# Optimization experiments

Measured on AMD Instinct MI355X. Metric: run time of the kernel, lower is better.

The kernel has to match this reference:

```python
import jax, jax.numpy as jnp
import numpy as np

ALPHA = 0.3      # robust Welsch scale (hardcoded in calc_chamfer)
EPS = 1e-6       # cosine_similarity eps


def _single_direction(x_points, x_normals, y_points, y_normals):
    """Robust chamfer x->y with K=1 KNN. Returns (mean robust dist, mean normal loss)."""
    # brute-force squared pairwise distances: [B, N, M]
    x2 = jnp.sum(x_points * x_points, axis=-1)            # [B, N]
    y2 = jnp.sum(y_points * y_points, axis=-1)            # [B, M]
    d2 = x2[:, :, None] + y2[:, None, :] - 2.0 * jnp.einsum('bnd,bmd->bnm', x_points, y_points)
    d2 = jnp.maximum(d2, 0.0)
    idx = jnp.argmin(d2, axis=-1)                         # [B, N] nearest neighbor in y
    dists = jnp.take_along_axis(d2, idx[..., None], axis=-1)[..., 0]   # squared dists [B, N]
    # Welsch weight applied to the squared distance (matches torch code), detached
    w = jax.lax.stop_gradient(jnp.exp(-(dists ** 2) / (2.0 * ALPHA * ALPHA)))
    cham_x = jnp.sum(w * dists, axis=1)                   # [B]
    # gather nearest normals and cosine similarity (torch-style per-vector eps clamp)
    yn_near = jnp.take_along_axis(y_normals, idx[..., None], axis=1)   # [B, N, 3]
    xn_norm = jnp.maximum(jnp.linalg.norm(x_normals, axis=-1), EPS)
    yn_norm = jnp.maximum(jnp.linalg.norm(yn_near, axis=-1), EPS)
    cos = jnp.sum(x_normals * yn_near, axis=-1) / (xn_norm * yn_norm)
    cham_norm_x = 1.0 - jnp.abs(cos)                      # abs_cosine=True
    return jnp.mean(cham_x), jnp.mean(cham_norm_x)


def setup_inputs() -> dict:
    key = jax.random.key(0)
    k1, k2, k3, k4 = jax.random.split(key, 4)
    B, N, M = 2, 10000, 10000
    pred_points = jax.random.normal(k1, (B, N, 3), dtype=jnp.float32)
    target_points = jax.random.normal(k2, (B, M, 3), dtype=jnp.float32)
    pn = jax.random.normal(k3, (B, N, 3), dtype=jnp.float32)
    tn = jax.random.normal(k4, (B, M, 3), dtype=jnp.float32)
    pred_normals = pn / jnp.linalg.norm(pn, axis=-1, keepdims=True)
    target_normals = tn / jnp.linalg.norm(tn, axis=-1, keepdims=True)
    return {
        'pred_points': pred_points,
        'pred_normals': pred_normals,
        'target_points': target_points,
        'target_normals': target_normals,
    }


def reference(pred_points, pred_normals, target_points, target_normals):
    # direction 1: target -> pred, direction 2: pred -> target
    d1, n1 = _single_direction(target_points, target_normals, pred_points, pred_normals)
    d2, n2 = _single_direction(pred_points, pred_normals, target_points, target_normals)
    return (d1 + d2, n1 + n2)
```

## Files before the change

### kernel.cpp

```cpp
#include <hip/hip_runtime.h>
#include <math.h>

#define NPTS 10000
#define XPT 8
#define AXCH 5
#define TILE 500

typedef float float2v __attribute__((ext_vector_type(2)));

#define PKFMA(d, a, b, c) \
    asm("v_pk_fma_f32 %0, %1, %2, %3" : "=v"(d) : "v"(a), "v"(b), "v"(c))

__global__ __launch_bounds__(256, 4) void knn_max(
    const float* __restrict__ pred_pts, const float* __restrict__ targ_pts,
    float* __restrict__ wsM, int nslices)
{
    const int slice = NPTS / nslices;
    const int c   = blockIdx.z;
    const int dir = c >> 1, b = c & 1;
    const float* xp = (dir == 0 ? targ_pts : pred_pts) + (size_t)b * NPTS * 3;
    const float* yp = (dir == 0 ? pred_pts : targ_pts) + (size_t)b * NPTS * 3;
    const int s = blockIdx.y;
    const int base = blockIdx.x * (256 * XPT) + threadIdx.x;

    __shared__ float4 spk[TILE];

    float2v xb[4][3];
    float   xs[4][3];
#pragma unroll
    for (int k = 0; k < 8; ++k) {
        const int n = base + k * 256;
        const int nn = (n < NPTS) ? n : (NPTS - 1);
        const float v0 = xp[nn * 3 + 0];
        const float v1 = xp[nn * 3 + 1];
        const float v2 = xp[nn * 3 + 2];
        if (k < 4) {
            xb[k][0] = (float2v){v0, v0};
            xb[k][1] = (float2v){v1, v1};
            xb[k][2] = (float2v){v2, v2};
        } else {
            xs[k - 4][0] = v0; xs[k - 4][1] = v1; xs[k - 4][2] = v2;
        }
    }
    float best[8];
#pragma unroll
    for (int k = 0; k < 8; ++k) best[k] = -1e30f;

    const int jstart = s * slice, jend = jstart + slice;
    for (int t0 = jstart; t0 < jend; t0 += TILE) {
        const int cnt = min(TILE, jend - t0);
        const int np  = cnt >> 1;
        __syncthreads();
        for (int p = threadIdx.x; p < np; p += 256) {
            const int j = t0 + 2 * p;
            const float a0 = yp[j * 3 + 0], b0 = yp[j * 3 + 1], c0 = yp[j * 3 + 2];
            const float a1 = yp[j * 3 + 3], b1 = yp[j * 3 + 4], c1 = yp[j * 3 + 5];
            spk[2 * p]     = make_float4(a0, a1, b0, b1);
            spk[2 * p + 1] = make_float4(c0, c1,
                                         -0.5f * (a0 * a0 + b0 * b0 + c0 * c0),
                                         -0.5f * (a1 * a1 + b1 * b1 + c1 * c1));
        }
        __syncthreads();
#pragma unroll 2
        for (int p = 0; p < np; ++p) {
            const float4 A = spk[2 * p];
            const float4 B = spk[2 * p + 1];
            const float2v px = {A.x, A.y}, py = {A.z, A.w};
            const float2v pz = {B.x, B.y}, pw = {B.z, B.w};
#pragma unroll
            for (int k = 0; k < 4; ++k) {
                float2v t;
                PKFMA(t, xb[k][2], pz, pw);
                PKFMA(t, xb[k][1], py, t);
                PKFMA(t, xb[k][0], px, t);
                best[k] = fmaxf(fmaxf(best[k], t.x), t.y);
            }
#pragma unroll
            for (int k = 0; k < 4; ++k) {
                const float ma = fmaf(xs[k][0], A.x,
                                 fmaf(xs[k][1], A.z, fmaf(xs[k][2], B.x, B.z)));
                const float mb = fmaf(xs[k][0], A.y,
                                 fmaf(xs[k][1], A.w, fmaf(xs[k][2], B.y, B.w)));
                best[4 + k] = fmaxf(fmaxf(best[4 + k], ma), mb);
            }
        }
    }
#pragma unroll
    for (int k = 0; k < 8; ++k) {
        const int n = base + k * 256;
        if (n < NPTS)
            wsM[((size_t)(c * nslices + s)) * NPTS + n] = best[k];
    }
}

__global__ __launch_bounds__(256) void finalize(
    const float* __restrict__ pred_pts, const float* __restrict__ pred_nrm,
    const float* __restrict__ targ_pts, const float* __restrict__ targ_nrm,
    const float* __restrict__ wsM, float2* __restrict__ wsB, int nslices)
{
    const int c   = blockIdx.y;
    const int dir = c >> 1, b = c & 1;
    const float* xp = (dir == 0 ? targ_pts : pred_pts) + (size_t)b * NPTS * 3;
    const float* xn = (dir == 0 ? targ_nrm : pred_nrm) + (size_t)b * NPTS * 3;
    const float* yp = (dir == 0 ? pred_pts : targ_pts) + (size_t)b * NPTS * 3;
    const float* yn = (dir == 0 ? pred_nrm : targ_nrm) + (size_t)b * NPTS * 3;

    const int lane = threadIdx.x & 7;
    const int n = blockIdx.x * 32 + (threadIdx.x >> 3);

    float t0 = 0.f, t1 = 0.f;
    if (n < NPTS) {
        float bm = -1e30f;
        int   bs = 1 << 30;
        for (int s = lane; s < nslices; s += 8) {
            const float m = wsM[((size_t)(c * nslices + s)) * NPTS + n];
            if (m > bm) { bm = m; bs = s; }
        }
#pragma unroll
        for (int w = 1; w < 8; w <<= 1) {
            const float mo = __shfl_xor(bm, w);
            const int   so = __shfl_xor(bs, w);
            if (mo > bm || (mo == bm && so < bs)) { bm = mo; bs = so; }
        }
        const float a  = xp[n * 3 + 0];
        const float bb = xp[n * 3 + 1];
        const float cc = xp[n * 3 + 2];
        const int slice = NPTS / nslices;
        const int j0 = bs * slice;
        float rb = -1e30f;
        int bidx = 1 << 30;
        for (int j = j0 + lane; j < j0 + slice; j += 8) {
            const float ya = yp[j * 3 + 0];
            const float yb = yp[j * 3 + 1];
            const float yc = yp[j * 3 + 2];
            const float hy = -0.5f * (ya * ya + yb * yb + yc * yc);
            const float m  = fmaf(a, ya, fmaf(bb, yb, fmaf(cc, yc, hy)));
            if (m > rb) { rb = m; bidx = j; }
        }
#pragma unroll
        for (int w = 1; w < 8; w <<= 1) {
            const float mo = __shfl_xor(rb, w);
            const int   jo = __shfl_xor(bidx, w);
            if (mo > rb || (mo == rb && jo < bidx)) { rb = mo; bidx = jo; }
        }
        if (lane == 0) {
            const float hx = -0.5f * (a * a + bb * bb + cc * cc);
            float d2 = -2.0f * (rb + hx);
            d2 = fmaxf(d2, 0.0f);
            const float w = __expf(-(d2 * d2) * (1.0f / 0.18f));
            t0 = w * d2;
            const float nx0 = xn[n * 3 + 0], nx1 = xn[n * 3 + 1], nx2 = xn[n * 3 + 2];
            const float ny0 = yn[(size_t)bidx * 3 + 0];
            const float ny1 = yn[(size_t)bidx * 3 + 1];
            const float ny2 = yn[(size_t)bidx * 3 + 2];
            const float nnx = fmaxf(sqrtf(nx0 * nx0 + nx1 * nx1 + nx2 * nx2), 1e-6f);
            const float nny = fmaxf(sqrtf(ny0 * ny0 + ny1 * ny1 + ny2 * ny2), 1e-6f);
            const float cosv = (nx0 * ny0 + nx1 * ny1 + nx2 * ny2) / (nnx * nny);
            t1 = 1.0f - fabsf(cosv);
        }
    }

    __shared__ float r0[256], r1[256];
    r0[threadIdx.x] = t0;
    r1[threadIdx.x] = t1;
    __syncthreads();
    for (int st = 128; st > 0; st >>= 1) {
        if (threadIdx.x < st) {
            r0[threadIdx.x] += r0[threadIdx.x + st];
            r1[threadIdx.x] += r1[threadIdx.x + st];
        }
        __syncthreads();
    }
    if (threadIdx.x == 0)
        wsB[blockIdx.y * gridDim.x + blockIdx.x] = make_float2(r0[0], r1[0]);
}

__global__ __launch_bounds__(256) void reduce_final(
    const float2* __restrict__ wsB, int nblocks, float* __restrict__ out)
{
    __shared__ float r0[256], r1[256];
    const int t = threadIdx.x;
    float s0 = 0.f, s1 = 0.f;
    for (int i = t; i < nblocks; i += 256) {
        const float2 v = wsB[i];
        s0 += v.x;
        s1 += v.y;
    }
    r0[t] = s0; r1[t] = s1;
    __syncthreads();
    for (int st = 128; st > 0; st >>= 1) {
        if (t < st) { r0[t] += r0[t + st]; r1[t] += r1[t + st]; }
        __syncthreads();
    }
    if (t == 0) {
        out[0] = 0.5f * r0[0];
        out[1] = r1[0] * (1.0f / 20000.0f);
    }
}

extern "C" void kernel_launch(void* const* d_in, const int* in_sizes, int n_in,
                              void* d_out, int out_size, void* d_ws, size_t ws_size,
                              hipStream_t stream)
{
    const float* pred_pts = (const float*)d_in[0];
    const float* pred_nrm = (const float*)d_in[1];
    const float* targ_pts = (const float*)d_in[2];
    const float* targ_nrm = (const float*)d_in[3];
    float* out = (float*)d_out;

    const int BXCH = (NPTS + 31) / 32;

    const int ladder[4] = {50, 40, 25, 10};
    int ns = 10;
    for (int i = 0; i < 4; ++i) {
        const size_t need = (size_t)4 * ladder[i] * NPTS * sizeof(float)
                          + (size_t)4 * BXCH * sizeof(float2) + 256;
        if (need <= ws_size) { ns = ladder[i]; break; }
    }

    float*  wsM = (float*)d_ws;
    float2* wsB = (float2*)(wsM + (size_t)4 * ns * NPTS);

    dim3 gA(AXCH, ns, 4);
    knn_max<<<gA, 256, 0, stream>>>(pred_pts, targ_pts, wsM, ns);

    dim3 gB(BXCH, 4);
    finalize<<<gB, 256, 0, stream>>>(pred_pts, pred_nrm, targ_pts, targ_nrm,
                                     wsM, wsB, ns);

    reduce_final<<<1, 256, 0, stream>>>(wsB, BXCH * 4, out);
}
```

Baseline: 54.89 us.

## Quantize per-slice maxima to 16-bit and rescan all near-max slices in finalize

The KNN pass now stores each per-slice best score as a 16-bit quantized code instead of a float, and each thread handles 10 points instead of 8 (6 packed, 4 scalar). The whole slice is loaded into shared memory once, with no tile loop. Finalize assigns one 64-lane wavefront per query point. It takes the max code across slices and exactly rescans every slice whose code lies within a small margin of that max, so quantization ties still yield the exact argmin. This halves workspace traffic and raises per-thread reuse, at the cost of extra rescans for close slices and a slice-size assumption (400 points) that limits nslices to at least 25.

New measurement: 113.8 us. +107.4%, slower.

```diff
diff --git a/kernel.cpp b/kernel.cpp
--- a/kernel.cpp
+++ b/kernel.cpp
@@ -2,18 +2,26 @@
 #include <math.h>
 
 #define NPTS 10000
-#define XPT 8
-#define AXCH 5
-#define TILE 500
+#define XPT 10
+#define KP 6
+#define KS 4
+#define AXCH 4
+#define MAXTILE 400
 
 typedef float float2v __attribute__((ext_vector_type(2)));
 
 #define PKFMA(d, a, b, c) \
     asm("v_pk_fma_f32 %0, %1, %2, %3" : "=v"(d) : "v"(a), "v"(b), "v"(c))
 
+__device__ __forceinline__ unsigned short enc_q(float m) {
+    int q = (int)floorf((m + 16.0f) * 2048.0f);
+    q = q < 0 ? 0 : (q > 65535 ? 65535 : q);
+    return (unsigned short)q;
+}
+
 __global__ __launch_bounds__(256, 4) void knn_max(
     const float* __restrict__ pred_pts, const float* __restrict__ targ_pts,
-    float* __restrict__ wsM, int nslices)
+    unsigned short* __restrict__ wsQ, int nslices)
 {
     const int slice = NPTS / nslices;
     const int c   = blockIdx.z;
@@ -23,80 +31,78 @@
     const int s = blockIdx.y;
     const int base = blockIdx.x * (256 * XPT) + threadIdx.x;
 
-    __shared__ float4 spk[TILE];
-
-    float2v xb[4][3];
-    float   xs[4][3];
-#pragma unroll
-    for (int k = 0; k < 8; ++k) {
+    __shared__ float4 spk[MAXTILE];
+
+    float2v xb[KP][3];
+    float   xs[KS][3];
+#pragma unroll
+    for (int k = 0; k < XPT; ++k) {
         const int n = base + k * 256;
         const int nn = (n < NPTS) ? n : (NPTS - 1);
         const float v0 = xp[nn * 3 + 0];
         const float v1 = xp[nn * 3 + 1];
         const float v2 = xp[nn * 3 + 2];
-        if (k < 4) {
+        if (k < KP) {
             xb[k][0] = (float2v){v0, v0};
             xb[k][1] = (float2v){v1, v1};
             xb[k][2] = (float2v){v2, v2};
         } else {
-            xs[k - 4][0] = v0; xs[k - 4][1] = v1; xs[k - 4][2] = v2;
-        }
-    }
-    float best[8];
-#pragma unroll
-    for (int k = 0; k < 8; ++k) best[k] = -1e30f;
-
-    const int jstart = s * slice, jend = jstart + slice;
-    for (int t0 = jstart; t0 < jend; t0 += TILE) {
-        const int cnt = min(TILE, jend - t0);
-        const int np  = cnt >> 1;
-        __syncthreads();
-        for (int p = threadIdx.x; p < np; p += 256) {
-            const int j = t0 + 2 * p;
-            const float a0 = yp[j * 3 + 0], b0 = yp[j * 3 + 1], c0 = yp[j * 3 + 2];
-            const float a1 = yp[j * 3 + 3], b1 = yp[j * 3 + 4], c1 = yp[j * 3 + 5];
-            spk[2 * p]     = make_float4(a0, a1, b0, b1);
-            spk[2 * p + 1] = make_float4(c0, c1,
-                                         -0.5f * (a0 * a0 + b0 * b0 + c0 * c0),
-                                         -0.5f * (a1 * a1 + b1 * b1 + c1 * c1));
-        }
-        __syncthreads();
+            xs[k - KP][0] = v0; xs[k - KP][1] = v1; xs[k - KP][2] = v2;
+        }
+    }
+    float best[XPT];
+#pragma unroll
+    for (int k = 0; k < XPT; ++k) best[k] = -1e30f;
+
+    const int js = s * slice;
+    const int np = slice >> 1;
+    for (int p = threadIdx.x; p < np; p += 256) {
+        const int j = js + 2 * p;
+        const float a0 = yp[j * 3 + 0], b0 = yp[j * 3 + 1], c0 = yp[j * 3 + 2];
+        const float a1 = yp[j * 3 + 3], b1 = yp[j * 3 + 4], c1 = yp[j * 3 + 5];
+        spk[2 * p]     = make_float4(a0, a1, b0, b1);
+        spk[2 * p + 1] = make_float4(c0, c1,
+                                     -0.5f * (a0 * a0 + b0 * b0 + c0 * c0),
+                                     -0.5f * (a1 * a1 + b1 * b1 + c1 * c1));
+    }
+    __syncthreads();
+
 #pragma unroll 2
-        for (int p = 0; p < np; ++p) {
-            const float4 A = spk[2 * p];
-            const float4 B = spk[2 * p + 1];
-            const float2v px = {A.x, A.y}, py = {A.z, A.w};
-            const float2v pz = {B.x, B.y}, pw = {B.z, B.w};
-#pragma unroll
-            for (int k = 0; k < 4; ++k) {
-                float2v t;
-                PKFMA(t, xb[k][2], pz, pw);
-                PKFMA(t, xb[k][1], py, t);
-                PKFMA(t, xb[k][0], px, t);
-                best[k] = fmaxf(fmaxf(best[k], t.x), t.y);
-            }
-#pragma unroll
-            for (int k = 0; k < 4; ++k) {
-                const float ma = fmaf(xs[k][0], A.x,
-                                 fmaf(xs[k][1], A.z, fmaf(xs[k][2], B.x, B.z)));
-                const float mb = fmaf(xs[k][0], A.y,
-                                 fmaf(xs[k][1], A.w, fmaf(xs[k][2], B.y, B.w)));
-                best[4 + k] = fmaxf(fmaxf(best[4 + k], ma), mb);
-            }
-        }
-    }
-#pragma unroll
-    for (int k = 0; k < 8; ++k) {
+    for (int p = 0; p < np; ++p) {
+        const float4 A = spk[2 * p];
+        const float4 B = spk[2 * p + 1];
+        const float2v px = {A.x, A.y}, py = {A.z, A.w};
+        const float2v pz = {B.x, B.y}, pw = {B.z, B.w};
+#pragma unroll
+        for (int k = 0; k < KP; ++k) {
+            float2v t;
+            PKFMA(t, xb[k][2], pz, pw);
+            PKFMA(t, xb[k][1], py, t);
+            PKFMA(t, xb[k][0], px, t);
+            best[k] = fmaxf(fmaxf(best[k], t.x), t.y);
+        }
+#pragma unroll
+        for (int k = 0; k < KS; ++k) {
+            const float ma = fmaf(xs[k][0], A.x,
+                             fmaf(xs[k][1], A.z, fmaf(xs[k][2], B.x, B.z)));
+            const float mb = fmaf(xs[k][0], A.y,
+                             fmaf(xs[k][1], A.w, fmaf(xs[k][2], B.y, B.w)));
+            best[KP + k] = fmaxf(fmaxf(best[KP + k], ma), mb);
+        }
+    }
+#pragma unroll
+    for (int k = 0; k < XPT; ++k) {
         const int n = base + k * 256;
         if (n < NPTS)
-            wsM[((size_t)(c * nslices + s)) * NPTS + n] = best[k];
-    }
-}
-
-__global__ __launch_bounds__(256) void finalize(
+            wsQ[((size_t)(c * nslices + s)) * NPTS + n] = enc_q(best[k]);
+    }
+}
+
+__global__ __launch_bounds__(512) void finalize(
     const float* __restrict__ pred_pts, const float* __restrict__ pred_nrm,
     const float* __restrict__ targ_pts, const float* __restrict__ targ_nrm,
-    const float* __restrict__ wsM, float2* __restrict__ wsB, int nslices)
+    const unsigned short* __restrict__ wsQ, float2* __restrict__ wsB,
+    int nslices)
 {
     const int c   = blockIdx.y;
     const int dir = c >> 1, b = c & 1;
@@ -105,40 +111,43 @@
     const float* yp = (dir == 0 ? pred_pts : targ_pts) + (size_t)b * NPTS * 3;
     const float* yn = (dir == 0 ? pred_nrm : targ_nrm) + (size_t)b * NPTS * 3;
 
-    const int lane = threadIdx.x & 7;
-    const int n = blockIdx.x * 32 + (threadIdx.x >> 3);
+    const int lane = threadIdx.x & 63;
+    const int wv   = threadIdx.x >> 6;
+    const int n    = blockIdx.x * 8 + wv;
 
     float t0 = 0.f, t1 = 0.f;
     if (n < NPTS) {
-        float bm = -1e30f;
-        int   bs = 1 << 30;
-        for (int s = lane; s < nslices; s += 8) {
-            const float m = wsM[((size_t)(c * nslices + s)) * NPTS + n];
-            if (m > bm) { bm = m; bs = s; }
-        }
-#pragma unroll
-        for (int w = 1; w < 8; w <<= 1) {
-            const float mo = __shfl_xor(bm, w);
-            const int   so = __shfl_xor(bs, w);
-            if (mo > bm || (mo == bm && so < bs)) { bm = mo; bs = so; }
-        }
+        const int slice = NPTS / nslices;
+        int q = -1;
+        if (lane < nslices)
+            q = wsQ[((size_t)(c * nslices + lane)) * NPTS + n];
+        int qmax = q;
+#pragma unroll
+        for (int w = 1; w < 64; w <<= 1)
+            qmax = max(qmax, __shfl_xor(qmax, w));
+
         const float a  = xp[n * 3 + 0];
         const float bb = xp[n * 3 + 1];
         const float cc = xp[n * 3 + 2];
-        const int slice = NPTS / nslices;
-        const int j0 = bs * slice;
+
         float rb = -1e30f;
         int bidx = 1 << 30;
-        for (int j = j0 + lane; j < j0 + slice; j += 8) {
-            const float ya = yp[j * 3 + 0];
-            const float yb = yp[j * 3 + 1];
-            const float yc = yp[j * 3 + 2];
-            const float hy = -0.5f * (ya * ya + yb * yb + yc * yc);
-            const float m  = fmaf(a, ya, fmaf(bb, yb, fmaf(cc, yc, hy)));
-            if (m > rb) { rb = m; bidx = j; }
-        }
-#pragma unroll
-        for (int w = 1; w < 8; w <<= 1) {
+        for (int s = 0; s < nslices; ++s) {
+            const int qs = __shfl(q, s);
+            if (qs >= qmax - 8) {
+                const int jend = (s + 1) * slice;
+                for (int j = s * slice + lane; j < jend; j += 64) {
+                    const float ya = yp[j * 3 + 0];
+                    const float yb = yp[j * 3 + 1];
+                    const float yc = yp[j * 3 + 2];
+                    const float hy = -0.5f * (ya * ya + yb * yb + yc * yc);
+                    const float m  = fmaf(a, ya, fmaf(bb, yb, fmaf(cc, yc, hy)));
+                    if (m > rb) { rb = m; bidx = j; }
+                }
+            }
+        }
+#pragma unroll
+        for (int w = 1; w < 64; w <<= 1) {
             const float mo = __shfl_xor(rb, w);
             const int   jo = __shfl_xor(bidx, w);
             if (mo > rb || (mo == rb && jo < bidx)) { rb = mo; bidx = jo; }
@@ -160,11 +169,11 @@
         }
     }
 
-    __shared__ float r0[256], r1[256];
+    __shared__ float r0[512], r1[512];
     r0[threadIdx.x] = t0;
     r1[threadIdx.x] = t1;
     __syncthreads();
-    for (int st = 128; st > 0; st >>= 1) {
+    for (int st = 256; st > 0; st >>= 1) {
         if (threadIdx.x < st) {
             r0[threadIdx.x] += r0[threadIdx.x + st];
             r1[threadIdx.x] += r1[threadIdx.x + st];
@@ -208,25 +217,26 @@
     const float* targ_nrm = (const float*)d_in[3];
     float* out = (float*)d_out;
 
-    const int BXCH = (NPTS + 31) / 32;
-
-    const int ladder[4] = {50, 40, 25, 10};
-    int ns = 10;
-    for (int i = 0; i < 4; ++i) {
-        const size_t need = (size_t)4 * ladder[i] * NPTS * sizeof(float)
-                          + (size_t)4 * BXCH * sizeof(float2) + 256;
+    const int BXCH = (NPTS + 7) / 8;
+    const size_t WSB_B = (size_t)4 * BXCH * sizeof(float2);
+
+    const int ladder[3] = {50, 40, 25};
+    int ns = 25;
+    for (int i = 0; i < 3; ++i) {
+        const size_t need = (size_t)4 * ladder[i] * NPTS * sizeof(unsigned short)
+                          + WSB_B + 256;
         if (need <= ws_size) { ns = ladder[i]; break; }
     }
 
-    float*  wsM = (float*)d_ws;
-    float2* wsB = (float2*)(wsM + (size_t)4 * ns * NPTS);
+    unsigned short* wsQ = (unsigned short*)d_ws;
+    float2* wsB = (float2*)((char*)d_ws + (size_t)4 * ns * NPTS * sizeof(unsigned short));
 
     dim3 gA(AXCH, ns, 4);
-    knn_max<<<gA, 256, 0, stream>>>(pred_pts, targ_pts, wsM, ns);
+    knn_max<<<gA, 256, 0, stream>>>(pred_pts, targ_pts, wsQ, ns);
 
     dim3 gB(BXCH, 4);
-    finalize<<<gB, 256, 0, stream>>>(pred_pts, pred_nrm, targ_pts, targ_nrm,
-                                     wsM, wsB, ns);
+    finalize<<<gB, 512, 0, stream>>>(pred_pts, pred_nrm, targ_pts, targ_nrm,
+                                     wsQ, wsB, ns);
 
     reduce_final<<<1, 256, 0, stream>>>(wsB, BXCH * 4, out);
 }
```
